# Performance work log

Measured on AMD Instinct MI355X. Metric: run time of the kernel, lower is better.

The kernel has to match this reference:

```python
import jax, jax.numpy as jnp
import numpy as np

BLOCK_SIZE = 256


def setup_inputs() -> dict:
    key = jax.random.key(0)
    k1, k2, k3, k4 = jax.random.split(key, 4)
    B, T, C, H = 128, BLOCK_SIZE, 1024, 128
    x = jax.random.normal(k1, (B, T, C), dtype=jnp.float32)
    # nn.Linear(C, H, bias=False): y = x @ W^T with W (H, C); we store W^T as (C, H)
    scale = 1.0 / np.sqrt(C)
    Wq = jax.random.uniform(k2, (C, H), dtype=jnp.float32, minval=-scale, maxval=scale)
    Wk = jax.random.uniform(k3, (C, H), dtype=jnp.float32, minval=-scale, maxval=scale)
    Wv = jax.random.uniform(k4, (C, H), dtype=jnp.float32, minval=-scale, maxval=scale)
    return {"x": x, "Wq": Wq, "Wk": Wk, "Wv": Wv}


def reference(x, Wq, Wk, Wv):
    B, T, C = x.shape
    Q = jnp.einsum('btc,ch->bth', x, Wq)
    K = jnp.einsum('btc,ch->bth', x, Wk)
    V = jnp.einsum('btc,ch->bth', x, Wv)
    d_k = Q.shape[-1]
    scores = jnp.einsum('bth,bsh->bts', Q, K) / jnp.sqrt(jnp.asarray(d_k, x.dtype))
    causal = jnp.tril(jnp.ones((T, T), dtype=bool))  # tril buffer
    scores = jnp.where(causal, scores, -jnp.inf)
    S = jax.nn.softmax(scores, axis=-1)
    out = jnp.einsum('bts,bsh->bth', S, V)
    return out
```

## Files before the change

### kernel.cpp

```cpp
#include <hip/hip_runtime.h>

typedef float  f32x4  __attribute__((ext_vector_type(4)));
typedef short  s16x8  __attribute__((ext_vector_type(8)));
typedef short  s16x4  __attribute__((ext_vector_type(4)));

__device__ __forceinline__ unsigned short f2bf(float f) {
    unsigned int u = __float_as_uint(f);
    return (unsigned short)((u + 0x7FFFu + ((u >> 16) & 1u)) >> 16);
}

__device__ __forceinline__ s16x8 cvt8(f32x4 a, f32x4 b) {
    union { unsigned int u[4]; s16x8 v; } r;
    asm("v_cvt_pk_bf16_f32 %0, %1, %2" : "=v"(r.u[0]) : "v"(a[0]), "v"(a[1]));
    asm("v_cvt_pk_bf16_f32 %0, %1, %2" : "=v"(r.u[1]) : "v"(a[2]), "v"(a[3]));
    asm("v_cvt_pk_bf16_f32 %0, %1, %2" : "=v"(r.u[2]) : "v"(b[0]), "v"(b[1]));
    asm("v_cvt_pk_bf16_f32 %0, %1, %2" : "=v"(r.u[3]) : "v"(b[2]), "v"(b[3]));
    return r.v;
}

__device__ __forceinline__ void lds_barrier() {
    asm volatile("s_waitcnt lgkmcnt(0)" ::: "memory");
    __builtin_amdgcn_s_barrier();
    asm volatile("" ::: "memory");
}

__global__ void prep_wt(const float* __restrict__ Wq,
                        const float* __restrict__ Wk,
                        const float* __restrict__ Wv,
                        unsigned short* __restrict__ wt) {
    int n = blockIdx.x;
    const float* W = (n < 128) ? Wq : ((n < 256) ? Wk : Wv);
    int h = n & 127;
    for (int k = threadIdx.x; k < 1024; k += blockDim.x) {
        wt[(size_t)n * 1024 + k] = f2bf(W[(size_t)k * 128 + h]);
    }
}

__global__ __launch_bounds__(512, 4) void qkv_gemm(
    const float* __restrict__ x,
    const unsigned short* __restrict__ wt,
    unsigned short* __restrict__ qo,
    unsigned short* __restrict__ ko,
    unsigned short* __restrict__ vto) {

    __shared__ char smem[57344];

    const int tid = threadIdx.x;
    const int bm  = blockIdx.x;
    const int lane = tid & 63, wid = tid >> 6;
    const int lm = lane & 15, l4 = lane >> 4;

    f32x4 acc[4][3];
#pragma unroll
    for (int i = 0; i < 4; ++i)
#pragma unroll
        for (int j = 0; j < 3; ++j) acc[i][j] = (f32x4)0.f;

    const int ar = tid >> 3;
    const float* xp = x + (size_t)(bm * 64 + ar) * 1024 + ((tid & 7) << 3);
    const int awr = ar * 128 + ((((tid & 7) << 4)) ^ ((ar & 7) << 4));

    int bgo[3], blw[3];
#pragma unroll
    for (int c = 0; c < 3; ++c) {
        int idx = c * 512 + tid;
        int row = idx >> 3;
        (void)row;
        bgo[c] = 0; blw[c] = 0;
    }
    int bgo6[6], blw6[6];
#pragma unroll
    for (int c = 0; c < 6; ++c) {
        int idx = c * 512 + tid;
        int row = idx >> 3;
        int c8  = idx & 7;
        bgo6[c] = row * 1024 + c8 * 8;
        blw6[c] = 8192 + row * 128 + ((c8 * 16) ^ ((row & 7) << 4));
    }

    int arow[4], brow[3];
#pragma unroll
    for (int mi = 0; mi < 4; ++mi) arow[mi] = mi * 16 + lm;
#pragma unroll
    for (int ni = 0; ni < 3; ++ni) brow[ni] = wid * 48 + ni * 16 + lm;

    f32x4 pa0 = *(const f32x4*)(xp);
    f32x4 pa1 = *(const f32x4*)(xp + 4);
    s16x8 pb[6];
#pragma unroll
    for (int c = 0; c < 6; ++c) pb[c] = *(const s16x8*)(wt + bgo6[c]);

    for (int ks = 0; ks < 16; ++ks) {
        lds_barrier();
        *(s16x8*)(smem + awr) = cvt8(pa0, pa1);
#pragma unroll
        for (int c = 0; c < 6; ++c) *(s16x8*)(smem + blw6[c]) = pb[c];
        lds_barrier();
        if (ks < 15) {
            pa0 = *(const f32x4*)(xp + (ks + 1) * 64);
            pa1 = *(const f32x4*)(xp + (ks + 1) * 64 + 4);
#pragma unroll
            for (int c = 0; c < 6; ++c)
                pb[c] = *(const s16x8*)(wt + bgo6[c] + (ks + 1) * 64);
        }
#pragma unroll
        for (int kkk = 0; kkk < 2; ++kkk) {
            s16x8 af[4], bf[3];
#pragma unroll
            for (int mi = 0; mi < 4; ++mi)
                af[mi] = *(const s16x8*)(smem + arow[mi] * 128 +
                           ((kkk * 64 + l4 * 16) ^ ((arow[mi] & 7) << 4)));
#pragma unroll
            for (int ni = 0; ni < 3; ++ni)
                bf[ni] = *(const s16x8*)(smem + 8192 + brow[ni] * 128 +
                           ((kkk * 64 + l4 * 16) ^ ((brow[ni] & 7) << 4)));
#pragma unroll
            for (int ni = 0; ni < 3; ++ni)
#pragma unroll
                for (int mi = 0; mi < 4; ++mi)
                    acc[mi][ni] = __builtin_amdgcn_mfma_f32_16x16x32_bf16(
                        af[mi], bf[ni], acc[mi][ni], 0, 0, 0);
        }
    }

#pragma unroll
    for (int mi = 0; mi < 4; ++mi) {
        int m0 = bm * 64 + mi * 16 + l4 * 4;
#pragma unroll
        for (int ni = 0; ni < 3; ++ni) {
            int nb  = wid * 48 + ni * 16;
            int mat = nb >> 7;
            int col = (nb & 127) + lm;
            if (mat == 2) {
                int bb = m0 >> 8, t = m0 & 255;
                s16x4 w4;
#pragma unroll
                for (int j = 0; j < 4; ++j) w4[j] = (short)f2bf(acc[mi][ni][j]);
                *(s16x4*)(vto + ((size_t)bb * 128 + col) * 256 + t) = w4;
            } else {
                unsigned short* dst = (mat == 0) ? qo : ko;
#pragma unroll
                for (int j = 0; j < 4; ++j)
                    dst[(size_t)(m0 + j) * 128 + col] = f2bf(acc[mi][ni][j]);
            }
        }
    }
}

__global__ __launch_bounds__(512) void attn(
    const unsigned short* __restrict__ q,
    const unsigned short* __restrict__ k,
    const unsigned short* __restrict__ vt,
    float* __restrict__ out) {

    __shared__ char pbuf[65536];

    const int tid = threadIdx.x, wid = tid >> 6, lane = tid & 63;
    const int lm = lane & 15, l4 = lane >> 4;
    const int b = blockIdx.x >> 1, qt = blockIdx.x & 1;
    const int qbase = qt << 7;
    const int t0 = qbase + wid * 16;
    const int nfrags = (qbase + 128) >> 4;
    const int nkf    = (qbase + 128) >> 5;

    const unsigned short* qrow = q + (size_t)(b * 256 + t0 + lm) * 128 + l4 * 8;
    s16x8 qf[4];
#pragma unroll
    for (int kf = 0; kf < 4; ++kf) qf[kf] = *(const s16x8*)(qrow + kf * 32);

    f32x4 sacc[16];
#pragma unroll
    for (int i = 0; i < 16; ++i) sacc[i] = (f32x4)0.f;

    const unsigned short* kbase = k + (size_t)(b * 256) * 128 + l4 * 8;
#pragma unroll
    for (int nf = 0; nf < 16; ++nf) {
        if (nf < nfrags) {
#pragma unroll
            for (int kf = 0; kf < 4; ++kf) {
                s16x8 a = *(const s16x8*)(kbase + (size_t)(nf * 16 + lm) * 128 + kf * 32);
                sacc[nf] = __builtin_amdgcn_mfma_f32_16x16x32_bf16(a, qf[kf], sacc[nf], 0, 0, 0);
            }
        }
    }

    const float scale = 0.08838834764831845f;
    const int tg = t0 + lm;
    float mx = -1e30f;
#pragma unroll
    for (int nf = 0; nf < 16; ++nf) {
        if (nf < nfrags) {
#pragma unroll
            for (int j = 0; j < 4; ++j) {
                int kv = nf * 16 + l4 * 4 + j;
                float s = sacc[nf][j] * scale;
                s = (kv > tg) ? -1e30f : s;
                sacc[nf][j] = s;
                mx = fmaxf(mx, s);
            }
        }
    }
    mx = fmaxf(mx, __shfl_xor(mx, 16));
    mx = fmaxf(mx, __shfl_xor(mx, 32));
    float sum = 0.f;
#pragma unroll
    for (int nf = 0; nf < 16; ++nf) {
        if (nf < nfrags) {
#pragma unroll
            for (int j = 0; j < 4; ++j) {
                float p = __expf(sacc[nf][j] - mx);
                sacc[nf][j] = p;
                sum += p;
            }
        }
    }
    sum += __shfl_xor(sum, 16);
    sum += __shfl_xor(sum, 32);
    float rinv = 1.0f / sum;

    char* pw = pbuf + wid * 8192 + lm * 512;
#pragma unroll
    for (int nf = 0; nf < 16; ++nf) {
        if (nf < nfrags) {
            s16x4 w;
#pragma unroll
            for (int j = 0; j < 4; ++j) w[j] = (short)f2bf(sacc[nf][j] * rinv);
            *(s16x4*)(pw + ((nf * 32 + l4 * 8) ^ ((lm & 7) << 4))) = w;
        }
    }
    asm volatile("s_waitcnt lgkmcnt(0)" ::: "memory");

    f32x4 oacc[8];
#pragma unroll
    for (int i = 0; i < 8; ++i) oacc[i] = (f32x4)0.f;

    const unsigned short* vbase = vt + (size_t)b * 32768 + l4 * 8;
#pragma unroll
    for (int kvf = 0; kvf < 8; ++kvf) {
        if (kvf < nkf) {
            s16x8 pf = *(const s16x8*)(pbuf + wid * 8192 + lm * 512 +
                        ((kvf * 64 + l4 * 16) ^ ((lm & 7) << 4)));
#pragma unroll
            for (int hf = 0; hf < 8; ++hf) {
                s16x8 a = *(const s16x8*)(vbase + (size_t)(hf * 16 + lm) * 256 + kvf * 32);
                oacc[hf] = __builtin_amdgcn_mfma_f32_16x16x32_bf16(a, pf, oacc[hf], 0, 0, 0);
            }
        }
    }

    float* ob = out + (size_t)(b * 256 + t0 + lm) * 128 + l4 * 4;
#pragma unroll
    for (int hf = 0; hf < 8; ++hf)
        *(f32x4*)(ob + hf * 16) = oacc[hf];
}

extern "C" void kernel_launch(void* const* d_in, const int* in_sizes, int n_in,
                              void* d_out, int out_size, void* d_ws, size_t ws_size,
                              hipStream_t stream) {
    const float* x  = (const float*)d_in[0];
    const float* Wq = (const float*)d_in[1];
    const float* Wk = (const float*)d_in[2];
    const float* Wv = (const float*)d_in[3];
    float* out = (float*)d_out;

    char* ws = (char*)d_ws;
    unsigned short* wt = (unsigned short*)(ws);
    unsigned short* qb = (unsigned short*)(ws + 786432);
    unsigned short* kb = (unsigned short*)(ws + 786432 + 8388608);
    unsigned short* vb = (unsigned short*)(ws + 786432 + 2 * 8388608);

    prep_wt<<<384, 256, 0, stream>>>(Wq, Wk, Wv, wt);
    qkv_gemm<<<512, 512, 0, stream>>>(x, wt, qb, kb, vb);
    attn<<<256, 512, 0, stream>>>(qb, kb, vb, out);
}
```

Measured before the change: 85.52 us.

## Load pre-swizzled weight fragments directly to registers and double-buffer the x tile

```diff
diff --git a/kernel.cpp b/kernel.cpp
--- a/kernel.cpp
+++ b/kernel.cpp
@@ -27,23 +27,29 @@
 __global__ void prep_wt(const float* __restrict__ Wq,
                         const float* __restrict__ Wk,
                         const float* __restrict__ Wv,
-                        unsigned short* __restrict__ wt) {
+                        unsigned char* __restrict__ wt3) {
     int n = blockIdx.x;
     const float* W = (n < 128) ? Wq : ((n < 256) ? Wk : Wv);
     int h = n & 127;
+    int n16 = n >> 4, lmn = n & 15;
     for (int k = threadIdx.x; k < 1024; k += blockDim.x) {
-        wt[(size_t)n * 1024 + k] = f2bf(W[(size_t)k * 128 + h]);
+        unsigned short v = f2bf(W[(size_t)k * 128 + h]);
+        int ks = k >> 6, rem = k & 63;
+        int kkk = rem >> 5, l4_ = (rem >> 3) & 3, j = rem & 7;
+        int lane = l4_ * 16 + lmn;
+        size_t off = (size_t)(n16 * 32 + ks * 2 + kkk) * 1024 + lane * 16 + j * 2;
+        *(unsigned short*)(wt3 + off) = v;
     }
 }
 
 __global__ __launch_bounds__(512, 4) void qkv_gemm(
     const float* __restrict__ x,
-    const unsigned short* __restrict__ wt,
+    const unsigned char* __restrict__ wt3,
     unsigned short* __restrict__ qo,
     unsigned short* __restrict__ ko,
     unsigned short* __restrict__ vto) {
 
-    __shared__ char smem[57344];
+    __shared__ char smem[16384];
 
     const int tid = threadIdx.x;
     const int bm  = blockIdx.x;
@@ -56,70 +62,78 @@
 #pragma unroll
         for (int j = 0; j < 3; ++j) acc[i][j] = (f32x4)0.f;
 
-    const int ar = tid >> 3;
-    const float* xp = x + (size_t)(bm * 64 + ar) * 1024 + ((tid & 7) << 3);
-    const int awr = ar * 128 + ((((tid & 7) << 4)) ^ ((ar & 7) << 4));
-
-    int bgo[3], blw[3];
-#pragma unroll
-    for (int c = 0; c < 3; ++c) {
-        int idx = c * 512 + tid;
-        int row = idx >> 3;
-        (void)row;
-        bgo[c] = 0; blw[c] = 0;
-    }
-    int bgo6[6], blw6[6];
-#pragma unroll
-    for (int c = 0; c < 6; ++c) {
-        int idx = c * 512 + tid;
-        int row = idx >> 3;
-        int c8  = idx & 7;
-        bgo6[c] = row * 1024 + c8 * 8;
-        blw6[c] = 8192 + row * 128 + ((c8 * 16) ^ ((row & 7) << 4));
-    }
-
-    int arow[4], brow[3];
+    const int ar  = tid >> 3;
+    const int ac8 = tid & 7;
+    const float* xp = x + (size_t)(bm * 64 + ar) * 1024 + ac8 * 8;
+    const int aw = ar * 128 + ((ac8 << 4) ^ ((ar & 7) << 4));
+
+    const unsigned char* wb = wt3 + (size_t)lane * 16;
+    int bqo[3];
+#pragma unroll
+    for (int ni = 0; ni < 3; ++ni) bqo[ni] = (wid * 3 + ni) * 32768;
+
+    int arow[4];
 #pragma unroll
     for (int mi = 0; mi < 4; ++mi) arow[mi] = mi * 16 + lm;
-#pragma unroll
-    for (int ni = 0; ni < 3; ++ni) brow[ni] = wid * 48 + ni * 16 + lm;
 
     f32x4 pa0 = *(const f32x4*)(xp);
     f32x4 pa1 = *(const f32x4*)(xp + 4);
-    s16x8 pb[6];
-#pragma unroll
-    for (int c = 0; c < 6; ++c) pb[c] = *(const s16x8*)(wt + bgo6[c]);
-
-    for (int ks = 0; ks < 16; ++ks) {
-        lds_barrier();
-        *(s16x8*)(smem + awr) = cvt8(pa0, pa1);
-#pragma unroll
-        for (int c = 0; c < 6; ++c) *(s16x8*)(smem + blw6[c]) = pb[c];
-        lds_barrier();
-        if (ks < 15) {
-            pa0 = *(const f32x4*)(xp + (ks + 1) * 64);
-            pa1 = *(const f32x4*)(xp + (ks + 1) * 64 + 4);
-#pragma unroll
-            for (int c = 0; c < 6; ++c)
-                pb[c] = *(const s16x8*)(wt + bgo6[c] + (ks + 1) * 64);
-        }
-#pragma unroll
-        for (int kkk = 0; kkk < 2; ++kkk) {
-            s16x8 af[4], bf[3];
+    s16x8 bq[6];
+#pragma unroll
+    for (int ni = 0; ni < 3; ++ni) {
+        bq[ni * 2]     = *(const s16x8*)(wb + bqo[ni]);
+        bq[ni * 2 + 1] = *(const s16x8*)(wb + bqo[ni] + 1024);
+    }
+    *(s16x8*)(smem + aw) = cvt8(pa0, pa1);
+    pa0 = *(const f32x4*)(xp + 64);
+    pa1 = *(const f32x4*)(xp + 68);
+    lds_barrier();
+
+    for (int t = 0; t < 16; ++t) {
+        const int ab = (t & 1) * 8192;
+        {
+            s16x8 af[4];
 #pragma unroll
             for (int mi = 0; mi < 4; ++mi)
-                af[mi] = *(const s16x8*)(smem + arow[mi] * 128 +
-                           ((kkk * 64 + l4 * 16) ^ ((arow[mi] & 7) << 4)));
-#pragma unroll
-            for (int ni = 0; ni < 3; ++ni)
-                bf[ni] = *(const s16x8*)(smem + 8192 + brow[ni] * 128 +
-                           ((kkk * 64 + l4 * 16) ^ ((brow[ni] & 7) << 4)));
+                af[mi] = *(const s16x8*)(smem + ab + arow[mi] * 128 +
+                           ((l4 * 16) ^ ((arow[mi] & 7) << 4)));
+            __builtin_amdgcn_s_setprio(1);
 #pragma unroll
             for (int ni = 0; ni < 3; ++ni)
 #pragma unroll
                 for (int mi = 0; mi < 4; ++mi)
                     acc[mi][ni] = __builtin_amdgcn_mfma_f32_16x16x32_bf16(
-                        af[mi], bf[ni], acc[mi][ni], 0, 0, 0);
+                        af[mi], bq[ni * 2], acc[mi][ni], 0, 0, 0);
+            __builtin_amdgcn_s_setprio(0);
+        }
+        {
+            s16x8 af[4];
+#pragma unroll
+            for (int mi = 0; mi < 4; ++mi)
+                af[mi] = *(const s16x8*)(smem + ab + arow[mi] * 128 +
+                           ((64 + l4 * 16) ^ ((arow[mi] & 7) << 4)));
+            __builtin_amdgcn_s_setprio(1);
+#pragma unroll
+            for (int ni = 0; ni < 3; ++ni)
+#pragma unroll
+                for (int mi = 0; mi < 4; ++mi)
+                    acc[mi][ni] = __builtin_amdgcn_mfma_f32_16x16x32_bf16(
+                        af[mi], bq[ni * 2 + 1], acc[mi][ni], 0, 0, 0);
+            __builtin_amdgcn_s_setprio(0);
+        }
+        if (t < 15) {
+            const unsigned char* wn = wb + (t + 1) * 2048;
+#pragma unroll
+            for (int ni = 0; ni < 3; ++ni) {
+                bq[ni * 2]     = *(const s16x8*)(wn + bqo[ni]);
+                bq[ni * 2 + 1] = *(const s16x8*)(wn + bqo[ni] + 1024);
+            }
+            *(s16x8*)(smem + (ab ^ 8192) + aw) = cvt8(pa0, pa1);
+            if (t < 14) {
+                pa0 = *(const f32x4*)(xp + (t + 2) * 64);
+                pa1 = *(const f32x4*)(xp + (t + 2) * 64 + 4);
+            }
+            lds_barrier();
         }
     }
 
@@ -132,11 +146,11 @@
             int mat = nb >> 7;
             int col = (nb & 127) + lm;
             if (mat == 2) {
-                int bb = m0 >> 8, t = m0 & 255;
+                int bb2 = m0 >> 8, tt = m0 & 255;
                 s16x4 w4;
 #pragma unroll
                 for (int j = 0; j < 4; ++j) w4[j] = (short)f2bf(acc[mi][ni][j]);
-                *(s16x4*)(vto + ((size_t)bb * 128 + col) * 256 + t) = w4;
+                *(s16x4*)(vto + ((size_t)bb2 * 128 + col) * 256 + tt) = w4;
             } else {
                 unsigned short* dst = (mat == 0) ? qo : ko;
 #pragma unroll
@@ -264,7 +278,7 @@
     float* out = (float*)d_out;
 
     char* ws = (char*)d_ws;
-    unsigned short* wt = (unsigned short*)(ws);
+    unsigned char*  wt = (unsigned char*)(ws);
     unsigned short* qb = (unsigned short*)(ws + 786432);
     unsigned short* kb = (unsigned short*)(ws + 786432 + 8388608);
     unsigned short* vb = (unsigned short*)(ws + 786432 + 2 * 8388608);
```

Measured after the change: 78.16 us. -8.6%, faster.
